# Kernel tuning notes

Measured on AMD Instinct MI355X. Metric: run time of the kernel, lower is better.

## Reference

```python
import jax, jax.numpy as jnp
import numpy as np

N = 12288      # nodes
E = 393216     # edges (avg degree 32)
IN = 256       # in_feats
H = 128        # n_hidden
DZ = 64        # dim_z


def setup_inputs() -> dict:
    key = jax.random.key(0)
    k = jax.random.split(key, 6)
    features = jax.random.normal(k[0], (N, IN), dtype=jnp.float32)
    edge_index = jax.random.randint(k[1], (2, E), 0, N, dtype=jnp.int64)
    # torch init is uniform(-1/sqrt(out), 1/sqrt(out)); scaled normal is fine for a numeric baseline
    W0 = jax.random.normal(k[2], (IN, H), dtype=jnp.float32) / np.float32(np.sqrt(H))
    Wm = jax.random.normal(k[3], (H, DZ), dtype=jnp.float32) / np.float32(np.sqrt(DZ))
    Ws = jax.random.normal(k[4], (H, DZ), dtype=jnp.float32) / np.float32(np.sqrt(DZ))
    noise = jax.random.normal(k[5], (N, DZ), dtype=jnp.float32)
    return {"features": features, "W0": W0, "Wm": Wm, "Ws": Ws,
            "noise": noise, "edge_index": edge_index}


def reference(features, W0, Wm, Ws, noise, edge_index):
    src, dst = edge_index[0], edge_index[1]
    n = features.shape[0]
    # symmetric degree norm (in-degree), as stored in g.ndata['norm']
    deg = jax.ops.segment_sum(jnp.ones((src.shape[0],), features.dtype), dst, num_segments=n)
    norm = (1.0 / jnp.sqrt(jnp.clip(deg, 1.0)))[:, None]  # [N,1]

    def gcn_layer(h, W, act):
        h = (h @ W) * norm                                   # dense matmul + pre-norm
        h = jax.ops.segment_sum(h[src], dst, num_segments=n)  # copy_src -> sum aggregation
        h = h * norm                                          # post-norm
        return act(h) if act is not None else h

    hidden = gcn_layer(features, W0, None)
    mean = gcn_layer(hidden, Wm, jax.nn.relu)
    logstd = gcn_layer(hidden, Ws, jax.nn.relu)
    Z = noise * jnp.exp(logstd) + mean   # reparameterization
    adj_logits = Z @ Z.T                 # [N, N]
    return adj_logits
```

## Files before the change

kernel.cpp:

```cpp
#include <hip/hip_runtime.h>
#include <math.h>

#define Nn 12288
#define Ee 393216
#define INF 256
#define Hh 128
#define DZ 64

__global__ void deg_kernel(const int* __restrict__ dst, float* __restrict__ deg) {
    int i = blockIdx.x * 256 + threadIdx.x;
    if (i < Ee) atomicAdd(&deg[dst[i]], 1.0f);
}

__global__ void norm_kernel(const float* __restrict__ deg, float* __restrict__ nrm) {
    int i = blockIdx.x * 256 + threadIdx.x;
    if (i < Nn) nrm[i] = 1.0f / sqrtf(fmaxf(deg[i], 1.0f));
}

__global__ __launch_bounds__(1024) void scan_kernel(const float* __restrict__ deg,
                                                    int* __restrict__ offs,
                                                    int* __restrict__ cursor) {
    __shared__ int part[1024];
    int t = threadIdx.x;
    int base = t * 12;
    int loc[12];
    int s = 0;
#pragma unroll
    for (int k = 0; k < 12; ++k) { loc[k] = s; s += (int)deg[base + k]; }
    part[t] = s;
    __syncthreads();
    for (int off = 1; off < 1024; off <<= 1) {
        int v = (t >= off) ? part[t - off] : 0;
        __syncthreads();
        part[t] += v;
        __syncthreads();
    }
    int pre = (t == 0) ? 0 : part[t - 1];
#pragma unroll
    for (int k = 0; k < 12; ++k) {
        int o = pre + loc[k];
        offs[base + k] = o;
        cursor[base + k] = o;
    }
    if (t == 1023) offs[Nn] = part[1023];
}

__global__ void csr_kernel(const int* __restrict__ src, const int* __restrict__ dst,
                           int* __restrict__ cursor, int* __restrict__ csr_src) {
    int e = blockIdx.x * 256 + threadIdx.x;
    if (e < Ee) {
        int p = atomicAdd(&cursor[dst[e]], 1);
        csr_src[p] = src[e];
    }
}

__global__ __launch_bounds__(128) void gemm1_kernel(const float* __restrict__ X,
                                                    const float* __restrict__ W0,
                                                    const float* __restrict__ nrm,
                                                    float* __restrict__ out) {
    __shared__ float xs[16][INF];
    int r0 = blockIdx.x * 16;
    int tid = threadIdx.x;
    const float4* X4 = (const float4*)(X + (size_t)r0 * INF);
    float4* xs4 = (float4*)&xs[0][0];
    for (int idx = tid; idx < 16 * INF / 4; idx += 128) xs4[idx] = X4[idx];
    __syncthreads();
    int j = tid;
    float acc[16];
#pragma unroll
    for (int r = 0; r < 16; ++r) acc[r] = 0.0f;
    for (int k = 0; k < INF; ++k) {
        float w = W0[k * Hh + j];
#pragma unroll
        for (int r = 0; r < 16; ++r) acc[r] += xs[r][k] * w;
    }
#pragma unroll
    for (int r = 0; r < 16; ++r) out[(size_t)(r0 + r) * Hh + j] = acc[r] * nrm[r0 + r];
}

__global__ __launch_bounds__(128) void agg1_kernel(const int* __restrict__ csr_src,
                                                   const int* __restrict__ offs,
                                                   const float* __restrict__ tmp1,
                                                   float* __restrict__ agg1) {
    __shared__ int sidx[128];
    int node = blockIdx.x;
    int beg = offs[node], end = offs[node + 1];
    int f = threadIdx.x;
    float acc = 0.0f;
    for (int e0 = beg; e0 < end; e0 += 128) {
        int n = min(128, end - e0);
        if (f < n) sidx[f] = csr_src[e0 + f];
        __syncthreads();
        for (int t = 0; t < n; ++t)
            acc += tmp1[(size_t)sidx[t] * Hh + f];
        __syncthreads();
    }
    agg1[(size_t)node * Hh + f] = acc;
}

__global__ __launch_bounds__(128) void gemm2_kernel(const float* __restrict__ agg1,
                                                    const float* __restrict__ Wm,
                                                    const float* __restrict__ Ws,
                                                    const float* __restrict__ nrm_g,
                                                    float* __restrict__ outm,
                                                    float* __restrict__ outs) {
    __shared__ float hs[16][Hh];
    __shared__ float nl[16];
    int r0 = blockIdx.x * 16;
    int tid = threadIdx.x;
    if (tid < 16) nl[tid] = nrm_g[r0 + tid];
    __syncthreads();
    for (int idx = tid; idx < 16 * Hh / 4; idx += 128) {
        int row = idx >> 5;
        float4 v = ((const float4*)agg1)[(size_t)r0 * (Hh / 4) + idx];
        float s = nl[row];
        v.x *= s; v.y *= s; v.z *= s; v.w *= s;
        ((float4*)&hs[0][0])[idx] = v;
    }
    __syncthreads();
    int j = tid & 63, sel = tid >> 6;
    const float* W = sel ? Ws : Wm;
    float* out = sel ? outs : outm;
    float acc[16];
#pragma unroll
    for (int r = 0; r < 16; ++r) acc[r] = 0.0f;
    for (int k = 0; k < Hh; ++k) {
        float w = W[k * DZ + j];
#pragma unroll
        for (int r = 0; r < 16; ++r) acc[r] += hs[r][k] * w;
    }
#pragma unroll
    for (int r = 0; r < 16; ++r) out[(size_t)(r0 + r) * DZ + j] = acc[r] * nl[r];
}

__global__ __launch_bounds__(128) void agg2_kernel(const int* __restrict__ csr_src,
                                                   const int* __restrict__ offs,
                                                   const float* __restrict__ tmpm,
                                                   const float* __restrict__ tmps,
                                                   float* __restrict__ aggm,
                                                   float* __restrict__ aggs) {
    __shared__ int sidx[128];
    int node = blockIdx.x;
    int beg = offs[node], end = offs[node + 1];
    int f = threadIdx.x & 63;
    const float* tin = (threadIdx.x >> 6) ? tmps : tmpm;
    float* tout = (threadIdx.x >> 6) ? aggs : aggm;
    float acc = 0.0f;
    for (int e0 = beg; e0 < end; e0 += 128) {
        int n = min(128, end - e0);
        if (threadIdx.x < n) sidx[threadIdx.x] = csr_src[e0 + threadIdx.x];
        __syncthreads();
        for (int t = 0; t < n; ++t)
            acc += tin[(size_t)sidx[t] * DZ + f];
        __syncthreads();
    }
    tout[(size_t)node * DZ + f] = acc;
}

__global__ void z_kernel(const float* __restrict__ aggm, const float* __restrict__ aggs,
                         const float* __restrict__ noise, const float* __restrict__ nrm,
                         float* __restrict__ Z) {
    int i = blockIdx.x * 256 + threadIdx.x;
    int node = i >> 6;
    float nr = nrm[node];
    float m = fmaxf(aggm[i] * nr, 0.0f);
    float s = fmaxf(aggs[i] * nr, 0.0f);
    Z[i] = noise[i] * expf(s) + m;
}

__global__ __launch_bounds__(256) void zzt_kernel(const float* __restrict__ Z,
                                                  float* __restrict__ out) {
    __shared__ float As[128 * 64];
    __shared__ float Bs[128 * 64];
    int i0 = blockIdx.y << 7, j0 = blockIdx.x << 7;
    int tid = threadIdx.x;

    for (int idx = tid; idx < 2048; idx += 256) {
        int row = idx >> 4;
        int c4 = idx & 15;
        int rot = (row >> 3) << 2;
        int cc = ((c4 << 2) + rot) & 63;
        float4 a = *(const float4*)(Z + ((size_t)(i0 + row) << 6) + (c4 << 2));
        float4 b = *(const float4*)(Z + ((size_t)(j0 + row) << 6) + (c4 << 2));
        *(float4*)&As[(row << 6) + cc] = a;
        *(float4*)&Bs[(row << 6) + cc] = b;
    }
    __syncthreads();

    int tx = tid & 15, ty = tid >> 4;
    float acc[8][8];
#pragma unroll
    for (int m = 0; m < 8; ++m)
#pragma unroll
        for (int n = 0; n < 8; ++n) acc[m][n] = 0.0f;

    int arot = ty << 2;
    int brot = tx << 2;
    const float* Abase = &As[(ty << 3) << 6];
    const float* Bbase = &Bs[(tx << 3) << 6];

    for (int k4 = 0; k4 < 16; ++k4) {
        int ka = ((k4 << 2) + arot) & 63;
        int kb = ((k4 << 2) + brot) & 63;
        float4 a4[8], b4[8];
#pragma unroll
        for (int m = 0; m < 8; ++m) a4[m] = *(const float4*)&Abase[(m << 6) + ka];
#pragma unroll
        for (int n = 0; n < 8; ++n) b4[n] = *(const float4*)&Bbase[(n << 6) + kb];
#pragma unroll
        for (int m = 0; m < 8; ++m)
#pragma unroll
            for (int n = 0; n < 8; ++n)
                acc[m][n] += a4[m].x * b4[n].x + a4[m].y * b4[n].y +
                             a4[m].z * b4[n].z + a4[m].w * b4[n].w;
    }

#pragma unroll
    for (int m = 0; m < 8; ++m) {
        size_t row = (size_t)(i0 + (ty << 3) + m);
        float4 v0 = {acc[m][0], acc[m][1], acc[m][2], acc[m][3]};
        float4 v1 = {acc[m][4], acc[m][5], acc[m][6], acc[m][7]};
        *(float4*)(out + row * Nn + j0 + (tx << 3)) = v0;
        *(float4*)(out + row * Nn + j0 + (tx << 3) + 4) = v1;
    }
}

extern "C" void kernel_launch(void* const* d_in, const int* in_sizes, int n_in,
                              void* d_out, int out_size, void* d_ws, size_t ws_size,
                              hipStream_t stream) {
    const float* X = (const float*)d_in[0];
    const float* W0 = (const float*)d_in[1];
    const float* Wm = (const float*)d_in[2];
    const float* Ws = (const float*)d_in[3];
    const float* noise = (const float*)d_in[4];
    const int* ei = (const int*)d_in[5];
    const int* srcp = ei;
    const int* dstp = ei + Ee;
    float* out = (float*)d_out;

    float* ws = (float*)d_ws;
    float* deg  = ws;
    float* agg1 = deg + Nn;
    float* aggm = agg1 + (size_t)Nn * Hh;
    float* aggs = aggm + (size_t)Nn * DZ;
    float* nrm  = aggs + (size_t)Nn * DZ;
    float* tmp1 = nrm + Nn;
    float* tmpm = tmp1 + (size_t)Nn * Hh;
    float* tmps = tmpm + (size_t)Nn * DZ;
    float* Zb   = tmps + (size_t)Nn * DZ;
    int* offs    = (int*)(Zb + (size_t)Nn * DZ);
    int* cursor  = offs + Nn + 1;
    int* csr_src = cursor + Nn;

    hipMemsetAsync(deg, 0, (size_t)Nn * sizeof(float), stream);

    deg_kernel<<<(Ee + 255) / 256, 256, 0, stream>>>(dstp, deg);
    norm_kernel<<<(Nn + 255) / 256, 256, 0, stream>>>(deg, nrm);
    scan_kernel<<<1, 1024, 0, stream>>>(deg, offs, cursor);
    csr_kernel<<<(Ee + 255) / 256, 256, 0, stream>>>(srcp, dstp, cursor, csr_src);
    gemm1_kernel<<<Nn / 16, 128, 0, stream>>>(X, W0, nrm, tmp1);
    agg1_kernel<<<Nn, 128, 0, stream>>>(csr_src, offs, tmp1, agg1);
    gemm2_kernel<<<Nn / 16, 128, 0, stream>>>(agg1, Wm, Ws, nrm, tmpm, tmps);
    agg2_kernel<<<Nn, 128, 0, stream>>>(csr_src, offs, tmpm, tmps, aggm, aggs);
    z_kernel<<<(Nn * DZ) / 256, 256, 0, stream>>>(aggm, aggs, noise, nrm, Zb);
    dim3 g(Nn / 128, Nn / 128);
    zzt_kernel<<<g, 256, 0, stream>>>(Zb, out);
}
```

Before: 919.6 us.

## Fuse norm into scan and Z into agg2, unroll gathers, use explicit FMAs

Computes the degree norm inside the scan kernel and folds the Z reparameterization into the second aggregation kernel, removing two launches and the aggm/aggs round trip through global memory. The gather loops are unrolled by four so several independent loads are in flight. The GEMM inner loops now use explicit fmaf, and the ZZ^T k-loop gets unroll 2, which may raise register pressure. Per-node summation order changes slightly.

```diff
diff --git a/kernel.cpp b/kernel.cpp
--- a/kernel.cpp
+++ b/kernel.cpp
@@ -12,21 +12,22 @@
     if (i < Ee) atomicAdd(&deg[dst[i]], 1.0f);
 }
 
-__global__ void norm_kernel(const float* __restrict__ deg, float* __restrict__ nrm) {
-    int i = blockIdx.x * 256 + threadIdx.x;
-    if (i < Nn) nrm[i] = 1.0f / sqrtf(fmaxf(deg[i], 1.0f));
-}
-
 __global__ __launch_bounds__(1024) void scan_kernel(const float* __restrict__ deg,
                                                     int* __restrict__ offs,
-                                                    int* __restrict__ cursor) {
+                                                    int* __restrict__ cursor,
+                                                    float* __restrict__ nrm) {
     __shared__ int part[1024];
     int t = threadIdx.x;
     int base = t * 12;
+    float dv[12];
     int loc[12];
     int s = 0;
 #pragma unroll
-    for (int k = 0; k < 12; ++k) { loc[k] = s; s += (int)deg[base + k]; }
+    for (int k = 0; k < 12; ++k) {
+        dv[k] = deg[base + k];
+        loc[k] = s;
+        s += (int)dv[k];
+    }
     part[t] = s;
     __syncthreads();
     for (int off = 1; off < 1024; off <<= 1) {
@@ -41,6 +42,7 @@
         int o = pre + loc[k];
         offs[base + k] = o;
         cursor[base + k] = o;
+        nrm[base + k] = 1.0f / sqrtf(fmaxf(dv[k], 1.0f));
     }
     if (t == 1023) offs[Nn] = part[1023];
 }
@@ -72,7 +74,7 @@
     for (int k = 0; k < INF; ++k) {
         float w = W0[k * Hh + j];
 #pragma unroll
-        for (int r = 0; r < 16; ++r) acc[r] += xs[r][k] * w;
+        for (int r = 0; r < 16; ++r) acc[r] = fmaf(xs[r][k], w, acc[r]);
     }
 #pragma unroll
     for (int r = 0; r < 16; ++r) out[(size_t)(r0 + r) * Hh + j] = acc[r] * nrm[r0 + r];
@@ -91,8 +93,16 @@
         int n = min(128, end - e0);
         if (f < n) sidx[f] = csr_src[e0 + f];
         __syncthreads();
-        for (int t = 0; t < n; ++t)
-            acc += tmp1[(size_t)sidx[t] * Hh + f];
+        int t = 0;
+        for (; t + 4 <= n; t += 4) {
+            int s0 = sidx[t], s1 = sidx[t + 1], s2 = sidx[t + 2], s3 = sidx[t + 3];
+            float v0 = tmp1[(size_t)s0 * Hh + f];
+            float v1 = tmp1[(size_t)s1 * Hh + f];
+            float v2 = tmp1[(size_t)s2 * Hh + f];
+            float v3 = tmp1[(size_t)s3 * Hh + f];
+            acc += (v0 + v1) + (v2 + v3);
+        }
+        for (; t < n; ++t) acc += tmp1[(size_t)sidx[t] * Hh + f];
         __syncthreads();
     }
     agg1[(size_t)node * Hh + f] = acc;
@@ -127,45 +137,51 @@
     for (int k = 0; k < Hh; ++k) {
         float w = W[k * DZ + j];
 #pragma unroll
-        for (int r = 0; r < 16; ++r) acc[r] += hs[r][k] * w;
+        for (int r = 0; r < 16; ++r) acc[r] = fmaf(hs[r][k], w, acc[r]);
     }
 #pragma unroll
     for (int r = 0; r < 16; ++r) out[(size_t)(r0 + r) * DZ + j] = acc[r] * nl[r];
 }
 
-__global__ __launch_bounds__(128) void agg2_kernel(const int* __restrict__ csr_src,
-                                                   const int* __restrict__ offs,
-                                                   const float* __restrict__ tmpm,
-                                                   const float* __restrict__ tmps,
-                                                   float* __restrict__ aggm,
-                                                   float* __restrict__ aggs) {
+__global__ __launch_bounds__(128) void agg2z_kernel(const int* __restrict__ csr_src,
+                                                    const int* __restrict__ offs,
+                                                    const float* __restrict__ tmpm,
+                                                    const float* __restrict__ tmps,
+                                                    const float* __restrict__ nrm,
+                                                    const float* __restrict__ noise,
+                                                    float* __restrict__ Z) {
     __shared__ int sidx[128];
+    __shared__ float sbuf[64];
     int node = blockIdx.x;
     int beg = offs[node], end = offs[node + 1];
     int f = threadIdx.x & 63;
     const float* tin = (threadIdx.x >> 6) ? tmps : tmpm;
-    float* tout = (threadIdx.x >> 6) ? aggs : aggm;
     float acc = 0.0f;
     for (int e0 = beg; e0 < end; e0 += 128) {
         int n = min(128, end - e0);
         if (threadIdx.x < n) sidx[threadIdx.x] = csr_src[e0 + threadIdx.x];
         __syncthreads();
-        for (int t = 0; t < n; ++t)
-            acc += tin[(size_t)sidx[t] * DZ + f];
-        __syncthreads();
-    }
-    tout[(size_t)node * DZ + f] = acc;
-}
-
-__global__ void z_kernel(const float* __restrict__ aggm, const float* __restrict__ aggs,
-                         const float* __restrict__ noise, const float* __restrict__ nrm,
-                         float* __restrict__ Z) {
-    int i = blockIdx.x * 256 + threadIdx.x;
-    int node = i >> 6;
-    float nr = nrm[node];
-    float m = fmaxf(aggm[i] * nr, 0.0f);
-    float s = fmaxf(aggs[i] * nr, 0.0f);
-    Z[i] = noise[i] * expf(s) + m;
+        int t = 0;
+        for (; t + 4 <= n; t += 4) {
+            int s0 = sidx[t], s1 = sidx[t + 1], s2 = sidx[t + 2], s3 = sidx[t + 3];
+            float v0 = tin[(size_t)s0 * DZ + f];
+            float v1 = tin[(size_t)s1 * DZ + f];
+            float v2 = tin[(size_t)s2 * DZ + f];
+            float v3 = tin[(size_t)s3 * DZ + f];
+            acc += (v0 + v1) + (v2 + v3);
+        }
+        for (; t < n; ++t) acc += tin[(size_t)sidx[t] * DZ + f];
+        __syncthreads();
+    }
+    if (threadIdx.x >= 64) sbuf[f] = acc;
+    __syncthreads();
+    if (threadIdx.x < 64) {
+        float nr = nrm[node];
+        float m = fmaxf(acc * nr, 0.0f);
+        float s = fmaxf(sbuf[f] * nr, 0.0f);
+        size_t i = (size_t)node * DZ + f;
+        Z[i] = fmaf(noise[i], expf(s), m);
+    }
 }
 
 __global__ __launch_bounds__(256) void zzt_kernel(const float* __restrict__ Z,
@@ -199,6 +215,7 @@
     const float* Abase = &As[(ty << 3) << 6];
     const float* Bbase = &Bs[(tx << 3) << 6];
 
+#pragma unroll 2
     for (int k4 = 0; k4 < 16; ++k4) {
         int ka = ((k4 << 2) + arot) & 63;
         int kb = ((k4 << 2) + brot) & 63;
@@ -211,8 +228,10 @@
         for (int m = 0; m < 8; ++m)
 #pragma unroll
             for (int n = 0; n < 8; ++n)
-                acc[m][n] += a4[m].x * b4[n].x + a4[m].y * b4[n].y +
-                             a4[m].z * b4[n].z + a4[m].w * b4[n].w;
+                acc[m][n] = fmaf(a4[m].w, b4[n].w,
+                            fmaf(a4[m].z, b4[n].z,
+                            fmaf(a4[m].y, b4[n].y,
+                            fmaf(a4[m].x, b4[n].x, acc[m][n]))));
     }
 
 #pragma unroll
@@ -241,9 +260,7 @@
     float* ws = (float*)d_ws;
     float* deg  = ws;
     float* agg1 = deg + Nn;
-    float* aggm = agg1 + (size_t)Nn * Hh;
-    float* aggs = aggm + (size_t)Nn * DZ;
-    float* nrm  = aggs + (size_t)Nn * DZ;
+    float* nrm  = agg1 + (size_t)Nn * Hh;
     float* tmp1 = nrm + Nn;
     float* tmpm = tmp1 + (size_t)Nn * Hh;
     float* tmps = tmpm + (size_t)Nn * DZ;
@@ -255,14 +272,12 @@
     hipMemsetAsync(deg, 0, (size_t)Nn * sizeof(float), stream);
 
     deg_kernel<<<(Ee + 255) / 256, 256, 0, stream>>>(dstp, deg);
-    norm_kernel<<<(Nn + 255) / 256, 256, 0, stream>>>(deg, nrm);
-    scan_kernel<<<1, 1024, 0, stream>>>(deg, offs, cursor);
+    scan_kernel<<<1, 1024, 0, stream>>>(deg, offs, cursor, nrm);
     csr_kernel<<<(Ee + 255) / 256, 256, 0, stream>>>(srcp, dstp, cursor, csr_src);
     gemm1_kernel<<<Nn / 16, 128, 0, stream>>>(X, W0, nrm, tmp1);
     agg1_kernel<<<Nn, 128, 0, stream>>>(csr_src, offs, tmp1, agg1);
     gemm2_kernel<<<Nn / 16, 128, 0, stream>>>(agg1, Wm, Ws, nrm, tmpm, tmps);
-    agg2_kernel<<<Nn, 128, 0, stream>>>(csr_src, offs, tmpm, tmps, aggm, aggs);
-    z_kernel<<<(Nn * DZ) / 256, 256, 0, stream>>>(aggm, aggs, noise, nrm, Zb);
+    agg2z_kernel<<<Nn, 128, 0, stream>>>(csr_src, offs, tmpm, tmps, nrm, noise, Zb);
     dim3 g(Nn / 128, Nn / 128);
     zzt_kernel<<<g, 256, 0, stream>>>(Zb, out);
 }
```

Result: faster. 898.7 us (-2.3%).
